# Performance work log

Measured on AMD Instinct MI355X. Metric: run time of the kernel, lower is better.

Reference implementation:

```python
import jax, jax.numpy as jnp
import numpy as np

B, T, N = 16, 32, 8192


def quaternion_to_matrix(q):
    # q: [..., 4] real-part-first (r, i, j, k); matches pytorch3d.quaternion_to_matrix
    r, i, j, k = q[..., 0], q[..., 1], q[..., 2], q[..., 3]
    two_s = 2.0 / jnp.sum(q * q, axis=-1)
    m = jnp.stack([
        1 - two_s * (j * j + k * k), two_s * (i * j - k * r), two_s * (i * k + j * r),
        two_s * (i * j + k * r), 1 - two_s * (i * i + k * k), two_s * (j * k - i * r),
        two_s * (i * k - j * r), two_s * (j * k + i * r), 1 - two_s * (i * i + j * j),
    ], axis=-1)
    return m.reshape(q.shape[:-1] + (3, 3))


def setup_inputs() -> dict:
    key = jax.random.key(0)
    k1, k2, k3, k4 = jax.random.split(key, 4)
    return {
        "pred": jax.random.normal(k1, (B, T, N, 3), dtype=jnp.float32),
        "cenp": jax.random.normal(k2, (B, T, N, 3), dtype=jnp.float32),
        "dofs": jax.random.normal(k3, (B, T, 4), dtype=jnp.float32),
        "ptrans": jax.random.normal(k4, (B, T, 3), dtype=jnp.float32),
    }


def reference(pred, cenp, dofs, ptrans):
    # R: [B, T, 3, 3]
    R = quaternion_to_matrix(dofs)
    points = pred - cenp                                   # [B,T,N,3]
    rotated = jnp.einsum('btni,btij->btnj', points, R)     # row-vector convention: points @ R
    # fused translate + recenter
    return rotated + ptrans[:, :, None, :] + cenp
```

## Files before the change

kernel.cpp:

```cpp
#include <hip/hip_runtime.h>
#include <hip/hip_bf16.h>


#define N_PTS 8192

__global__ __launch_bounds__(256) void tooth_assembler_kernel(
    const float* __restrict__ pred,
    const float* __restrict__ cenp,
    const float* __restrict__ dofs,
    const float* __restrict__ ptrans,
    float* __restrict__ out,
    int total_groups)
{
    int g = blockIdx.x * blockDim.x + threadIdx.x;
    if (g >= total_groups) return;

    int pt0 = g * 4;
    int bt  = pt0 >> 13;

    const float4 q = *reinterpret_cast<const float4*>(dofs + bt * 4);
    float r = q.x, i = q.y, j = q.z, k = q.w;
    float two_s = 2.0f / (r * r + i * i + j * j + k * k);
    float R00 = 1.0f - two_s * (j * j + k * k);
    float R01 = two_s * (i * j - k * r);
    float R02 = two_s * (i * k + j * r);
    float R10 = two_s * (i * j + k * r);
    float R11 = 1.0f - two_s * (i * i + k * k);
    float R12 = two_s * (j * k - i * r);
    float R20 = two_s * (i * k - j * r);
    float R21 = two_s * (j * k + i * r);
    float R22 = 1.0f - two_s * (i * i + j * j);

    float tx = ptrans[bt * 3 + 0];
    float ty = ptrans[bt * 3 + 1];
    float tz = ptrans[bt * 3 + 2];

    size_t base = (size_t)pt0 * 3;
    const float4* pp = reinterpret_cast<const float4*>(pred + base);
    const float4* cc = reinterpret_cast<const float4*>(cenp + base);
    float4 p0 = pp[0], p1 = pp[1], p2 = pp[2];
    float4 c0 = cc[0], c1 = cc[1], c2 = cc[2];

    float pf[12] = {p0.x, p0.y, p0.z, p0.w, p1.x, p1.y, p1.z, p1.w, p2.x, p2.y, p2.z, p2.w};
    float cf[12] = {c0.x, c0.y, c0.z, c0.w, c1.x, c1.y, c1.z, c1.w, c2.x, c2.y, c2.z, c2.w};
    float of[12];

#pragma unroll
    for (int m = 0; m < 4; ++m) {
        float x = pf[3 * m + 0] - cf[3 * m + 0];
        float y = pf[3 * m + 1] - cf[3 * m + 1];
        float z = pf[3 * m + 2] - cf[3 * m + 2];
        of[3 * m + 0] = x * R00 + y * R10 + z * R20 + tx + cf[3 * m + 0];
        of[3 * m + 1] = x * R01 + y * R11 + z * R21 + ty + cf[3 * m + 1];
        of[3 * m + 2] = x * R02 + y * R12 + z * R22 + tz + cf[3 * m + 2];
    }

    float4* oo = reinterpret_cast<float4*>(out + base);
    oo[0] = make_float4(of[0], of[1], of[2], of[3]);
    oo[1] = make_float4(of[4], of[5], of[6], of[7]);
    oo[2] = make_float4(of[8], of[9], of[10], of[11]);
}

extern "C" void kernel_launch(void* const* d_in, const int* in_sizes, int n_in,
                              void* d_out, int out_size, void* d_ws, size_t ws_size,
                              hipStream_t stream) {
    const float* pred   = (const float*)d_in[0];
    const float* cenp   = (const float*)d_in[1];
    const float* dofs   = (const float*)d_in[2];
    const float* ptrans = (const float*)d_in[3];
    float* out = (float*)d_out;

    int total_points = in_sizes[0] / 3;
    int total_groups = total_points / 4;
    int block = 256;
    int grid = (total_groups + block - 1) / block;

    tooth_assembler_kernel<<<grid, block, 0, stream>>>(pred, cenp, dofs, ptrans, out, total_groups);
}
```

Measured before the change: 137.8 us.

## Stage tiles through shared memory with coalesced float4 loads in a grid-stride loop

Each block now loads a tile of 1024 points from pred and cenp into LDS with fully coalesced float4 accesses, transforms the points in LDS, and writes the results back with coalesced float4 stores. A persistent grid of 2048 blocks walks the tiles in a grid-stride loop. The goal is to replace the stride-3 float4 accesses per thread with contiguous per-wavefront accesses. The cost is three barriers per tile, LDS traffic with stride-3 bank patterns, and a fixed grid size that may leave the GPU underfilled or unbalanced.

```diff
diff --git a/kernel.cpp b/kernel.cpp
--- a/kernel.cpp
+++ b/kernel.cpp
@@ -2,7 +2,11 @@
 #include <hip/hip_bf16.h>
 
 
-#define N_PTS 8192
+#define BLOCK 256
+#define PTS_PER_THREAD 4
+#define TILE_PTS (BLOCK * PTS_PER_THREAD)
+#define TILE_F (TILE_PTS * 3)
+#define TILE_F4 (TILE_F / 4)
 
 __global__ __launch_bounds__(256) void tooth_assembler_kernel(
     const float* __restrict__ pred,
@@ -10,55 +14,63 @@
     const float* __restrict__ dofs,
     const float* __restrict__ ptrans,
     float* __restrict__ out,
-    int total_groups)
+    int n_tiles)
 {
-    int g = blockIdx.x * blockDim.x + threadIdx.x;
-    if (g >= total_groups) return;
+    __shared__ float sp[TILE_F];
+    __shared__ float sc[TILE_F];
 
-    int pt0 = g * 4;
-    int bt  = pt0 >> 13;
+    const int tid = threadIdx.x;
+    float4* sp4 = reinterpret_cast<float4*>(sp);
+    float4* sc4 = reinterpret_cast<float4*>(sc);
 
-    const float4 q = *reinterpret_cast<const float4*>(dofs + bt * 4);
-    float r = q.x, i = q.y, j = q.z, k = q.w;
-    float two_s = 2.0f / (r * r + i * i + j * j + k * k);
-    float R00 = 1.0f - two_s * (j * j + k * k);
-    float R01 = two_s * (i * j - k * r);
-    float R02 = two_s * (i * k + j * r);
-    float R10 = two_s * (i * j + k * r);
-    float R11 = 1.0f - two_s * (i * i + k * k);
-    float R12 = two_s * (j * k - i * r);
-    float R20 = two_s * (i * k - j * r);
-    float R21 = two_s * (j * k + i * r);
-    float R22 = 1.0f - two_s * (i * i + j * j);
+    for (int tile = blockIdx.x; tile < n_tiles; tile += gridDim.x) {
+        int bt = tile >> 3;
 
-    float tx = ptrans[bt * 3 + 0];
-    float ty = ptrans[bt * 3 + 1];
-    float tz = ptrans[bt * 3 + 2];
+        const float4 q = *reinterpret_cast<const float4*>(dofs + bt * 4);
+        float r = q.x, i = q.y, j = q.z, k = q.w;
+        float two_s = 2.0f / (r * r + i * i + j * j + k * k);
+        float R00 = 1.0f - two_s * (j * j + k * k);
+        float R01 = two_s * (i * j - k * r);
+        float R02 = two_s * (i * k + j * r);
+        float R10 = two_s * (i * j + k * r);
+        float R11 = 1.0f - two_s * (i * i + k * k);
+        float R12 = two_s * (j * k - i * r);
+        float R20 = two_s * (i * k - j * r);
+        float R21 = two_s * (j * k + i * r);
+        float R22 = 1.0f - two_s * (i * i + j * j);
+        float tx = ptrans[bt * 3 + 0];
+        float ty = ptrans[bt * 3 + 1];
+        float tz = ptrans[bt * 3 + 2];
 
-    size_t base = (size_t)pt0 * 3;
-    const float4* pp = reinterpret_cast<const float4*>(pred + base);
-    const float4* cc = reinterpret_cast<const float4*>(cenp + base);
-    float4 p0 = pp[0], p1 = pp[1], p2 = pp[2];
-    float4 c0 = cc[0], c1 = cc[1], c2 = cc[2];
-
-    float pf[12] = {p0.x, p0.y, p0.z, p0.w, p1.x, p1.y, p1.z, p1.w, p2.x, p2.y, p2.z, p2.w};
-    float cf[12] = {c0.x, c0.y, c0.z, c0.w, c1.x, c1.y, c1.z, c1.w, c2.x, c2.y, c2.z, c2.w};
-    float of[12];
+        size_t base4 = (size_t)tile * TILE_F4;
+        const float4* p4 = reinterpret_cast<const float4*>(pred) + base4;
+        const float4* c4 = reinterpret_cast<const float4*>(cenp) + base4;
+        float4* o4 = reinterpret_cast<float4*>(out) + base4;
 
 #pragma unroll
-    for (int m = 0; m < 4; ++m) {
-        float x = pf[3 * m + 0] - cf[3 * m + 0];
-        float y = pf[3 * m + 1] - cf[3 * m + 1];
-        float z = pf[3 * m + 2] - cf[3 * m + 2];
-        of[3 * m + 0] = x * R00 + y * R10 + z * R20 + tx + cf[3 * m + 0];
-        of[3 * m + 1] = x * R01 + y * R11 + z * R21 + ty + cf[3 * m + 1];
-        of[3 * m + 2] = x * R02 + y * R12 + z * R22 + tz + cf[3 * m + 2];
+        for (int s = 0; s < 3; ++s) {
+            sp4[tid + BLOCK * s] = p4[tid + BLOCK * s];
+            sc4[tid + BLOCK * s] = c4[tid + BLOCK * s];
+        }
+        __syncthreads();
+
+#pragma unroll
+        for (int m = 0; m < PTS_PER_THREAD; ++m) {
+            int e = 3 * (tid + BLOCK * m);
+            float cx = sc[e], cy = sc[e + 1], cz = sc[e + 2];
+            float x = sp[e] - cx, y = sp[e + 1] - cy, z = sp[e + 2] - cz;
+            sp[e]     = x * R00 + y * R10 + z * R20 + tx + cx;
+            sp[e + 1] = x * R01 + y * R11 + z * R21 + ty + cy;
+            sp[e + 2] = x * R02 + y * R12 + z * R22 + tz + cz;
+        }
+        __syncthreads();
+
+#pragma unroll
+        for (int s = 0; s < 3; ++s) {
+            o4[tid + BLOCK * s] = sp4[tid + BLOCK * s];
+        }
+        __syncthreads();
     }
-
-    float4* oo = reinterpret_cast<float4*>(out + base);
-    oo[0] = make_float4(of[0], of[1], of[2], of[3]);
-    oo[1] = make_float4(of[4], of[5], of[6], of[7]);
-    oo[2] = make_float4(of[8], of[9], of[10], of[11]);
 }
 
 extern "C" void kernel_launch(void* const* d_in, const int* in_sizes, int n_in,
@@ -71,9 +83,8 @@
     float* out = (float*)d_out;
 
     int total_points = in_sizes[0] / 3;
-    int total_groups = total_points / 4;
-    int block = 256;
-    int grid = (total_groups + block - 1) / block;
+    int n_tiles = total_points / TILE_PTS;
+    int grid = 2048;
 
-    tooth_assembler_kernel<<<grid, block, 0, stream>>>(pred, cenp, dofs, ptrans, out, total_groups);
+    tooth_assembler_kernel<<<grid, BLOCK, 0, stream>>>(pred, cenp, dofs, ptrans, out, n_tiles);
 }
```

Result: no change. 139.5 us (+1.3%).
